# Performance work log

Hardware: AMD Instinct MI355X
Metric: run time of the kernel (lower is better)

The kernel has to match this reference:

```python
import jax, jax.numpy as jnp
import numpy as np

N_NODES = 100000
N_EDGES = 1600000
EMB = 64       # embedding_dim
HID = 128      # hidden_channels
N_GRAPHS = 512
N_TASKS = 128
ATOM_VOCAB = 119
BOND_VOCAB = 16


def setup_inputs() -> dict:
    key = jax.random.key(0)
    ks = jax.random.split(key, 24)
    s = 0.02
    inp = {
        'x_idx': jax.random.randint(ks[0], (N_NODES,), 0, ATOM_VOCAB),
        'edge_index': jax.random.randint(ks[1], (2, N_EDGES), 0, N_NODES),
        'edge_attr_idx': jax.random.randint(ks[2], (N_EDGES,), 0, BOND_VOCAB),
        'batch': jnp.sort(jax.random.randint(ks[3], (N_NODES,), 0, N_GRAPHS)),
        'atom_emb': jax.random.normal(ks[4], (ATOM_VOCAB, EMB), jnp.float32) * s,
        'bond_emb': jax.random.normal(ks[5], (BOND_VOCAB, EMB), jnp.float32) * s,
        'w_edge0': jax.random.normal(ks[6], (EMB, EMB), jnp.float32) * s,
        'b_edge0': jnp.zeros((EMB,), jnp.float32),
        'w1_0': jax.random.normal(ks[7], (EMB, HID), jnp.float32) * s,
        'b1_0': jnp.zeros((HID,), jnp.float32),
        'w2_0': jax.random.normal(ks[8], (HID, HID), jnp.float32) * s,
        'b2_0': jnp.zeros((HID,), jnp.float32),
        'w_edge1': jax.random.normal(ks[9], (EMB, HID), jnp.float32) * s,
        'b_edge1': jnp.zeros((HID,), jnp.float32),
        'w1_1': jax.random.normal(ks[10], (HID, HID), jnp.float32) * s,
        'b1_1': jnp.zeros((HID,), jnp.float32),
        'w2_1': jax.random.normal(ks[11], (HID, HID), jnp.float32) * s,
        'b2_1': jnp.zeros((HID,), jnp.float32),
        'lin1_w': jax.random.normal(ks[12], (HID, HID), jnp.float32) * s,
        'lin1_b': jnp.zeros((HID,), jnp.float32),
        'lin2_w': jax.random.normal(ks[13], (HID, N_TASKS), jnp.float32) * s,
        'lin2_b': jnp.zeros((N_TASKS,), jnp.float32),
    }
    return inp


def _gine_conv(x, e, src, dst, we, be, w1, b1, w2, b2):
    # message: relu(x_j + Linear(edge_attr)); aggregate: scatter-add at dst
    msg = jax.nn.relu(x[src] + e @ we + be)            # [E, in_dim]
    agg = jax.ops.segment_sum(msg, dst, num_segments=N_NODES)
    h = x + agg                                        # (1+eps)*x with eps=0
    h = jax.nn.elu(h @ w1 + b1) @ w2 + b2              # GINE nn MLP
    return jax.nn.elu(h)                               # outer F.elu


def reference(x_idx, edge_index, edge_attr_idx, batch,
              atom_emb, bond_emb,
              w_edge0, b_edge0, w1_0, b1_0, w2_0, b2_0,
              w_edge1, b_edge1, w1_1, b1_1, w2_1, b2_1,
              lin1_w, lin1_b, lin2_w, lin2_b):
    x = atom_emb[x_idx]                                # [N, EMB]
    e = bond_emb[edge_attr_idx]                        # [E, EMB]
    src, dst = edge_index[0], edge_index[1]            # flow: source->target
    x = _gine_conv(x, e, src, dst, w_edge0, b_edge0, w1_0, b1_0, w2_0, b2_0)
    x = _gine_conv(x, e, src, dst, w_edge1, b_edge1, w1_1, b1_1, w2_1, b2_1)
    hg = jax.ops.segment_sum(x, batch, num_segments=N_GRAPHS)  # global_add_pool
    hg = jax.nn.relu(hg @ lin1_w + lin1_b)
    return hg @ lin2_w + lin2_b                        # [G, num_tasks]
```

## Files before the change

kernel.cpp:

```cpp
#include <hip/hip_runtime.h>
#include <hip/hip_bf16.h>

static const int NN = 100000;
static const int NE = 1600000;
static const int NG = 512;
static const int NB = 391;
static const int PS = 4608;
static const int CS = 6400;

typedef __attribute__((ext_vector_type(8))) short shortx8;
typedef __attribute__((ext_vector_type(4))) float floatx4;
typedef __attribute__((ext_vector_type(2))) float floatx2;

__device__ __forceinline__ float bf2f(unsigned short u) {
  union { unsigned int i; float f; } v; v.i = ((unsigned int)u) << 16; return v.f;
}
__device__ __forceinline__ unsigned short f2bf(float f) {
  union { float f; unsigned int i; } v; v.f = f;
  return (unsigned short)((v.i + 0x7FFFu + ((v.i >> 16) & 1u)) >> 16);
}
__device__ __forceinline__ float elu_fast(float v) {
  return v > 0.f ? v : (__builtin_amdgcn_exp2f(v * 1.44269504f) - 1.f);
}
__device__ __forceinline__ floatx2 unpk(unsigned int v) {
  union { unsigned int i; float f; } a, b;
  a.i = v << 16; b.i = v & 0xFFFF0000u;
  floatx2 r; r.x = a.f; r.y = b.f; return r;
}

__global__ void k_prep(const float* __restrict__ bond,
                       const float* __restrict__ we0, const float* __restrict__ be0,
                       const float* __restrict__ we1, const float* __restrict__ be1,
                       const float* __restrict__ atom,
                       float* __restrict__ et1, unsigned short* __restrict__ M0,
                       float* __restrict__ hgf, int* __restrict__ bcursor,
                       unsigned short* __restrict__ x1s,
                       const float* __restrict__ s0, const float* __restrict__ s1,
                       const float* __restrict__ s2, const float* __restrict__ s3,
                       const float* __restrict__ s4, const float* __restrict__ s5,
                       unsigned short* __restrict__ d0, unsigned short* __restrict__ d1,
                       unsigned short* __restrict__ d2, unsigned short* __restrict__ d3,
                       unsigned short* __restrict__ d4, unsigned short* __restrict__ d5) {
  int blk = blockIdx.x, t = threadIdx.x;
  if (blk < 8) {
    int i = blk * 256 + t;
    int b = i >> 7, c = i & 127;
    float acc = be1[c];
    for (int k = 0; k < 64; ++k) acc += bond[b * 64 + k] * we1[k * 128 + c];
    et1[i] = acc;
  } else if (blk < 484) {
    int i = (blk - 8) * 256 + t;
    int c = i & 63, b = (i >> 6) & 15, a = i >> 10;
    float acc = be0[c];
    for (int k = 0; k < 64; ++k) acc += bond[b * 64 + k] * we0[k * 64 + c];
    acc += atom[a * 64 + c];
    M0[i] = f2bf(acc > 0.f ? acc : 0.f);
  } else if (blk < 868) {
    int task = (blk - 484) >> 6;
    int i = ((blk - 484) & 63) * 256 + t;
    const float* w; unsigned short* wz; int K;
    switch (task) {
      case 0: w = s0; wz = d0; K = 64; break;
      case 1: w = s1; wz = d1; K = 128; break;
      case 2: w = s2; wz = d2; K = 128; break;
      case 3: w = s3; wz = d3; K = 128; break;
      case 4: w = s4; wz = d4; K = 128; break;
      default: w = s5; wz = d5; K = 128; break;
    }
    if (i >= K * 128) return;
    int j = i & 7, lane = (i >> 3) & 63, ct = (i >> 9) & 7, s = i >> 12;
    int k = s * 32 + (lane >> 4) * 8 + j;
    int m = ct * 16 + (lane & 15);
    wz[i] = f2bf(w[k * 128 + m]);
  } else if (blk < 884) {
    int base = (blk - 868) * 4096;
#pragma unroll
    for (int k = 0; k < 16; ++k) hgf[base + k * 256 + t] = 0.f;
  } else {
    if (t < NB) bcursor[t] = t * PS;
    int u = t + 256;
    if (u < NB) bcursor[u] = u * PS;
    if (t < 32) ((unsigned int*)(M0 + 1904 * 64))[t] = 0u;
    if (t < 64) ((unsigned int*)(x1s + (size_t)NN * 128))[t] = 0xFF80FF80u;
  }
}

__global__ void k_bin(const int* __restrict__ src, const int* __restrict__ dstp,
                      const int* __restrict__ ea, const int* __restrict__ x_idx,
                      int* __restrict__ bcursor, uint2* __restrict__ pairs) {
  __shared__ int cnt[512];
  __shared__ int incl[512];
  __shared__ int cur[NB];
  __shared__ int rbase[NB];
  __shared__ uint2 stage[4096];
  int t = threadIdx.x;
  int e0 = blockIdx.x * 4096;
  int ecnt = NE - e0; if (ecnt > 4096) ecnt = 4096;
  cnt[t] = 0; cnt[t + 256] = 0;
  __syncthreads();
  for (int k = 0; k < 16; ++k) {
    int i = k * 256 + t;
    if (i < ecnt) atomicAdd(&cnt[dstp[e0 + i] >> 8], 1);
  }
  __syncthreads();
  incl[t] = cnt[t]; incl[t + 256] = cnt[t + 256];
  __syncthreads();
  for (int d = 1; d < 512; d <<= 1) {
    int v0 = (t >= d) ? incl[t - d] : 0;
    int v1 = (t + 256 >= d) ? incl[t + 256 - d] : 0;
    __syncthreads();
    incl[t] += v0; incl[t + 256] += v1;
    __syncthreads();
  }
  if (t < NB) { cur[t] = incl[t] - cnt[t]; if (cnt[t]) rbase[t] = atomicAdd(&bcursor[t], cnt[t]); }
  int u = t + 256;
  if (u < NB) { cur[u] = incl[u] - cnt[u]; if (cnt[u]) rbase[u] = atomicAdd(&bcursor[u], cnt[u]); }
  __syncthreads();
  for (int k = 0; k < 16; ++k) {
    int i = k * 256 + t;
    if (i < ecnt) {
      int e = e0 + i;
      int d = dstp[e];
      int s = src[e];
      unsigned int pk = (unsigned int)s | ((unsigned int)(x_idx[s] * 16 + ea[e]) << 17);
      int p = atomicAdd(&cur[d >> 8], 1);
      stage[p] = make_uint2((unsigned int)d, pk);
    }
  }
  __syncthreads();
  for (int j = t; j < ecnt; j += 256) {
    uint2 p = stage[j];
    int b = (int)(p.x >> 8);
    int excl = incl[b] - cnt[b];
    pairs[rbase[b] + (j - excl)] = p;
  }
}

__global__ void k_fine(const uint2* __restrict__ pairs, const int* __restrict__ bcursor,
                       int* __restrict__ offs, int* __restrict__ cnts,
                       unsigned int* __restrict__ csr0, unsigned int* __restrict__ csr1) {
  __shared__ int cnt[256];
  __shared__ int incl[256];
  __shared__ int cur[256];
  int b = blockIdx.x;
  int t = threadIdx.x;
  int start = b * PS;
  int endv = bcursor[b];
  int cbase = b * CS;
  int base_n = b << 8;
  cnt[t] = 0;
  __syncthreads();
  for (int j = start + t; j < endv; j += 256)
    atomicAdd(&cnt[(int)pairs[j].x - base_n], 1);
  __syncthreads();
  int myc = cnt[t];
  int myp = (myc + 7) & ~7;
  incl[t] = myp;
  __syncthreads();
  for (int d = 1; d < 256; d <<= 1) {
    int v = (t >= d) ? incl[t - d] : 0;
    __syncthreads();
    incl[t] += v;
    __syncthreads();
  }
  int excl = incl[t] - myp;
  cur[t] = excl;
  int node = base_n + t;
  if (node < NN) { offs[node] = cbase + excl; cnts[node] = myc; }
  __syncthreads();
  for (int j = start + t; j < endv; j += 256) {
    uint2 p = pairs[j];
    int pos = cbase + atomicAdd(&cur[(int)p.x - base_n], 1);
    unsigned int pk = p.y;
    unsigned int idx17 = pk >> 17;
    csr0[pos] = idx17 << 7;
    csr1[pos] = ((pk & 0x1FFFFu) << 8) | (idx17 & 15u);
  }
  __syncthreads();
  for (int j = myc; j < myp; ++j) {
    int pos = cbase + excl + j;
    csr0[pos] = (unsigned int)(1904 << 7);
    csr1[pos] = ((unsigned int)NN) << 8;
  }
}

__global__ __launch_bounds__(256) void k_agg0(
    const int* __restrict__ x_idx, const float* __restrict__ atom,
    const unsigned short* __restrict__ M0, const int* __restrict__ offs,
    const int* __restrict__ cnts,
    const unsigned int* __restrict__ csr0, unsigned short* __restrict__ h0) {
  int t = threadIdx.x, lane = t & 63;
  int half = lane >> 5, c = lane & 31;
  int n = __builtin_amdgcn_readfirstlane(blockIdx.x * 4 + (t >> 6));
  if (n >= NN) return;
  int s = offs[n];
  int ep = s + ((cnts[n] + 7) & ~7);
  const char* Mb = (const char*)M0;
  unsigned int voff = (unsigned int)c * 4u;
  floatx2 acc; acc.x = 0.f; acc.y = 0.f;
  if (half == 0) {
    float2 sv = *(const float2*)((const char*)atom +
                                 ((size_t)(unsigned)x_idx[n] << 8) + (size_t)c * 8u);
    acc.x = sv.x; acc.y = sv.y;
  }
  for (int i = s; i < ep; i += 8) {
    unsigned int a0 = csr0[i + 0], b0 = csr0[i + 1];
    unsigned int a1 = csr0[i + 2], b1 = csr0[i + 3];
    unsigned int a2 = csr0[i + 4], b2 = csr0[i + 5];
    unsigned int a3 = csr0[i + 6], b3 = csr0[i + 7];
    unsigned int q0 = half ? b0 : a0, q1 = half ? b1 : a1;
    unsigned int q2 = half ? b2 : a2, q3 = half ? b3 : a3;
    unsigned int v0 = *(const unsigned int*)(Mb + q0 + voff);
    unsigned int v1 = *(const unsigned int*)(Mb + q1 + voff);
    unsigned int v2 = *(const unsigned int*)(Mb + q2 + voff);
    unsigned int v3 = *(const unsigned int*)(Mb + q3 + voff);
    acc = acc + unpk(v0);
    acc = acc + unpk(v1);
    acc = acc + unpk(v2);
    acc = acc + unpk(v3);
  }
  float ax = acc.x + __shfl_xor(acc.x, 32);
  float ay = acc.y + __shfl_xor(acc.y, 32);
  if (half == 0) {
    unsigned int o = (unsigned int)f2bf(ax) | ((unsigned int)f2bf(ay) << 16);
    *(unsigned int*)(h0 + (size_t)n * 64 + c * 2) = o;
  }
}

__global__ __launch_bounds__(256) void k_agg1(
    const unsigned short* __restrict__ x1, const float* __restrict__ et1,
    const int* __restrict__ offs, const int* __restrict__ cnts,
    const unsigned int* __restrict__ csr1, unsigned short* __restrict__ h1) {
  __shared__ float etl[2048];
  int t = threadIdx.x;
#pragma unroll
  for (int k = 0; k < 8; ++k) etl[k * 256 + t] = et1[k * 256 + t];
  __syncthreads();
  int lane = t & 63;
  int n = __builtin_amdgcn_readfirstlane(blockIdx.x * 4 + (t >> 6));
  if (n >= NN) return;
  int s = offs[n];
  int ep = s + ((cnts[n] + 7) & ~7);
  const char* xb = (const char*)x1;
  unsigned int voff = (unsigned int)lane * 4u;
  const char* etb = (const char*)etl + (size_t)lane * 8u;
  unsigned int xv = *(const unsigned int*)(xb + ((size_t)(unsigned)n << 8) + voff);
  floatx2 acc = unpk(xv);
  floatx2 zero2; zero2.x = 0.f; zero2.y = 0.f;
  for (int i = s; i < ep; i += 8) {
    unsigned int q0 = csr1[i + 0], q1 = csr1[i + 1], q2 = csr1[i + 2], q3 = csr1[i + 3];
    unsigned int q4 = csr1[i + 4], q5 = csr1[i + 5], q6 = csr1[i + 6], q7 = csr1[i + 7];
    unsigned int v0 = *(const unsigned int*)(xb + ((q0 & 0xFFFFFF00u) | voff));
    unsigned int v1 = *(const unsigned int*)(xb + ((q1 & 0xFFFFFF00u) | voff));
    unsigned int v2 = *(const unsigned int*)(xb + ((q2 & 0xFFFFFF00u) | voff));
    unsigned int v3 = *(const unsigned int*)(xb + ((q3 & 0xFFFFFF00u) | voff));
    unsigned int v4 = *(const unsigned int*)(xb + ((q4 & 0xFFFFFF00u) | voff));
    unsigned int v5 = *(const unsigned int*)(xb + ((q5 & 0xFFFFFF00u) | voff));
    unsigned int v6 = *(const unsigned int*)(xb + ((q6 & 0xFFFFFF00u) | voff));
    unsigned int v7 = *(const unsigned int*)(xb + ((q7 & 0xFFFFFF00u) | voff));
    floatx2 e0 = *(const floatx2*)(etb + ((q0 & 15u) << 9));
    floatx2 e1 = *(const floatx2*)(etb + ((q1 & 15u) << 9));
    floatx2 e2 = *(const floatx2*)(etb + ((q2 & 15u) << 9));
    floatx2 e3 = *(const floatx2*)(etb + ((q3 & 15u) << 9));
    floatx2 e4 = *(const floatx2*)(etb + ((q4 & 15u) << 9));
    floatx2 e5 = *(const floatx2*)(etb + ((q5 & 15u) << 9));
    floatx2 e6 = *(const floatx2*)(etb + ((q6 & 15u) << 9));
    floatx2 e7 = *(const floatx2*)(etb + ((q7 & 15u) << 9));
    acc = acc + __builtin_elementwise_max(unpk(v0) + e0, zero2);
    acc = acc + __builtin_elementwise_max(unpk(v1) + e1, zero2);
    acc = acc + __builtin_elementwise_max(unpk(v2) + e2, zero2);
    acc = acc + __builtin_elementwise_max(unpk(v3) + e3, zero2);
    acc = acc + __builtin_elementwise_max(unpk(v4) + e4, zero2);
    acc = acc + __builtin_elementwise_max(unpk(v5) + e5, zero2);
    acc = acc + __builtin_elementwise_max(unpk(v6) + e6, zero2);
    acc = acc + __builtin_elementwise_max(unpk(v7) + e7, zero2);
  }
  unsigned int o = (unsigned int)f2bf(acc.x) | ((unsigned int)f2bf(acc.y) << 16);
  *(unsigned int*)(h1 + (size_t)n * 128 + lane * 2) = o;
}

template <int K1>
__global__ __launch_bounds__(256) void k_mlp_t(
    const unsigned short* __restrict__ in,
    const unsigned short* __restrict__ w1z, const float* __restrict__ b1,
    const unsigned short* __restrict__ w2z, const float* __restrict__ b2,
    unsigned short* __restrict__ outb, int N) {
  __shared__ unsigned short tls[4][16][136];
  __shared__ unsigned short b2s[16384];
  int t = threadIdx.x;
  int lane = t & 63;
  int wave = t >> 6;
  int rlo = lane & 15, quad = lane >> 4;

#pragma unroll
  for (int k = 0; k < 8; ++k)
    *(shortx8*)&b2s[(k * 256 + t) * 8] = *(const shortx8*)&w2z[(k * 256 + t) * 8];

  float bm1[8], bm2[8];
#pragma unroll
  for (int ct = 0; ct < 8; ++ct) { bm1[ct] = b1[ct * 16 + rlo]; bm2[ct] = b2[ct * 16 + rlo]; }

  __syncthreads();

#pragma unroll
  for (int t2 = 0; t2 < 2; ++t2) {
    int row0 = blockIdx.x * 128 + t2 * 64 + wave * 16;
    int arow = row0 + rlo;

    floatx4 acc[8];
#pragma unroll
    for (int ct = 0; ct < 8; ++ct) { acc[ct][0]=0.f; acc[ct][1]=0.f; acc[ct][2]=0.f; acc[ct][3]=0.f; }
    const int NS = K1 >> 5;
#pragma unroll
    for (int s = 0; s < NS; ++s) {
      shortx8 a = {0,0,0,0,0,0,0,0};
      if (arow < N) a = *(const shortx8*)(in + (size_t)arow * K1 + s * 32 + quad * 8);
      const unsigned short* wp = w1z + ((size_t)(s * 8) * 64 + lane) * 8;
#pragma unroll
      for (int ct = 0; ct < 8; ++ct) {
        shortx8 b = *(const shortx8*)(wp + ct * 512);
        acc[ct] = __builtin_amdgcn_mfma_f32_16x16x32_bf16(a, b, acc[ct], 0, 0, 0);
      }
    }
#pragma unroll
    for (int ct = 0; ct < 8; ++ct) {
#pragma unroll
      for (int r = 0; r < 4; ++r) {
        float v = elu_fast(acc[ct][r] + bm1[ct]);
        tls[wave][quad * 4 + r][ct * 16 + rlo] = f2bf(v);
      }
    }

    floatx4 acc2[8];
#pragma unroll
    for (int ct = 0; ct < 8; ++ct) { acc2[ct][0]=0.f; acc2[ct][1]=0.f; acc2[ct][2]=0.f; acc2[ct][3]=0.f; }
#pragma unroll
    for (int s = 0; s < 4; ++s) {
      shortx8 a = *(const shortx8*)&tls[wave][rlo][s * 32 + quad * 8];
      const unsigned short* wp = &b2s[((s * 8) * 64 + lane) * 8];
#pragma unroll
      for (int ct = 0; ct < 8; ++ct) {
        shortx8 b = *(const shortx8*)(wp + ct * 512);
        acc2[ct] = __builtin_amdgcn_mfma_f32_16x16x32_bf16(a, b, acc2[ct], 0, 0, 0);
      }
    }
#pragma unroll
    for (int ct = 0; ct < 8; ++ct) {
#pragma unroll
      for (int r = 0; r < 4; ++r) {
        float v = elu_fast(acc2[ct][r] + bm2[ct]);
        tls[wave][quad * 4 + r][ct * 16 + rlo] = f2bf(v);
      }
    }
    int srow = lane >> 2;
    int schunk = lane & 3;
    int grow = row0 + srow;
#pragma unroll
    for (int k = 0; k < 4; ++k) {
      int ch = schunk + k * 4;
      if (grow < N)
        *(shortx8*)(outb + (size_t)grow * 128 + ch * 8) =
            *(const shortx8*)&tls[wave][srow][ch * 8];
    }
  }
}

__global__ __launch_bounds__(256) void k_pool(
    const unsigned short* __restrict__ x2, const int* __restrict__ batch,
    float* __restrict__ hgf) {
  int gt = blockIdx.x * 256 + threadIdx.x;
  int chunk = gt >> 6, lane = gt & 63;
  int n0 = chunk * 32;
  if (n0 >= NN) return;
  int nend = n0 + 32; if (nend > NN) nend = NN;
  float ax = 0.f, ay = 0.f;
  const unsigned short* xp = x2 + lane * 2;
  int gcur = batch[n0];
  for (int n = n0; n < nend; ++n) {
    int g = batch[n];
    if (g != gcur) {
      atomicAdd(&hgf[gcur * 128 + lane * 2], ax);
      atomicAdd(&hgf[gcur * 128 + lane * 2 + 1], ay);
      ax = 0.f; ay = 0.f; gcur = g;
    }
    unsigned int v = *(const unsigned int*)(xp + (size_t)n * 128);
    ax += bf2f((unsigned short)(v & 0xFFFF));
    ay += bf2f((unsigned short)(v >> 16));
  }
  atomicAdd(&hgf[gcur * 128 + lane * 2], ax);
  atomicAdd(&hgf[gcur * 128 + lane * 2 + 1], ay);
}

__global__ void k_head(const float* __restrict__ in,
                       const unsigned short* __restrict__ w1z, const float* __restrict__ b1,
                       const unsigned short* __restrict__ w2z, const float* __restrict__ b2,
                       float* __restrict__ outf, int N) {
  __shared__ unsigned short tls[4][16][136];
  int lane = threadIdx.x & 63;
  int wave = threadIdx.x >> 6;
  int row0 = blockIdx.x * 64 + wave * 16;
  int rlo = lane & 15, quad = lane >> 4;
  int arow = row0 + rlo;
  floatx4 acc[8];
#pragma unroll
  for (int ct = 0; ct < 8; ++ct) { acc[ct][0]=0.f; acc[ct][1]=0.f; acc[ct][2]=0.f; acc[ct][3]=0.f; }
#pragma unroll
  for (int s = 0; s < 4; ++s) {
    shortx8 a = {0,0,0,0,0,0,0,0};
    if (arow < N) {
      const float* rp = in + (size_t)arow * 128 + s * 32 + quad * 8;
      float4 f0 = *(const float4*)rp;
      float4 f1 = *(const float4*)(rp + 4);
      a[0] = (short)f2bf(f0.x); a[1] = (short)f2bf(f0.y);
      a[2] = (short)f2bf(f0.z); a[3] = (short)f2bf(f0.w);
      a[4] = (short)f2bf(f1.x); a[5] = (short)f2bf(f1.y);
      a[6] = (short)f2bf(f1.z); a[7] = (short)f2bf(f1.w);
    }
    const unsigned short* wp = w1z + ((size_t)(s * 8) * 64 + lane) * 8;
#pragma unroll
    for (int ct = 0; ct < 8; ++ct) {
      shortx8 b = *(const shortx8*)(wp + ct * 512);
      acc[ct] = __builtin_amdgcn_mfma_f32_16x16x32_bf16(a, b, acc[ct], 0, 0, 0);
    }
  }
#pragma unroll
  for (int ct = 0; ct < 8; ++ct) {
    float bm = b1[ct * 16 + rlo];
#pragma unroll
    for (int r = 0; r < 4; ++r) {
      float v = acc[ct][r] + bm;
      v = v > 0.f ? v : 0.f;
      tls[wave][quad * 4 + r][ct * 16 + rlo] = f2bf(v);
    }
  }
  __syncthreads();
  floatx4 acc2[8];
#pragma unroll
  for (int ct = 0; ct < 8; ++ct) { acc2[ct][0]=0.f; acc2[ct][1]=0.f; acc2[ct][2]=0.f; acc2[ct][3]=0.f; }
#pragma unroll
  for (int s = 0; s < 4; ++s) {
    shortx8 a = *(const shortx8*)&tls[wave][rlo][s * 32 + quad * 8];
    const unsigned short* wp = w2z + ((size_t)(s * 8) * 64 + lane) * 8;
#pragma unroll
    for (int ct = 0; ct < 8; ++ct) {
      shortx8 b = *(const shortx8*)(wp + ct * 512);
      acc2[ct] = __builtin_amdgcn_mfma_f32_16x16x32_bf16(a, b, acc2[ct], 0, 0, 0);
    }
  }
#pragma unroll
  for (int ct = 0; ct < 8; ++ct) {
    float bm = b2[ct * 16 + rlo];
#pragma unroll
    for (int r = 0; r < 4; ++r) {
      int rr = row0 + quad * 4 + r;
      if (rr < N) outf[(size_t)rr * 128 + ct * 16 + rlo] = acc2[ct][r] + bm;
    }
  }
}

extern "C" void kernel_launch(void* const* d_in, const int* in_sizes, int n_in,
                              void* d_out, int out_size, void* d_ws, size_t ws_size,
                              hipStream_t stream) {
  const int* x_idx  = (const int*)d_in[0];
  const int* e_src  = (const int*)d_in[1];
  const int* e_dst  = e_src + NE;
  const int* e_attr = (const int*)d_in[2];
  const int* batch  = (const int*)d_in[3];
  const float* atom = (const float*)d_in[4];
  const float* bond = (const float*)d_in[5];
  const float* we0  = (const float*)d_in[6];
  const float* be0  = (const float*)d_in[7];
  const float* w1_0 = (const float*)d_in[8];
  const float* b1_0 = (const float*)d_in[9];
  const float* w2_0 = (const float*)d_in[10];
  const float* b2_0 = (const float*)d_in[11];
  const float* we1  = (const float*)d_in[12];
  const float* be1  = (const float*)d_in[13];
  const float* w1_1 = (const float*)d_in[14];
  const float* b1_1 = (const float*)d_in[15];
  const float* w2_1 = (const float*)d_in[16];
  const float* b2_1 = (const float*)d_in[17];
  const float* l1w  = (const float*)d_in[18];
  const float* l1b  = (const float*)d_in[19];
  const float* l2w  = (const float*)d_in[20];
  const float* l2b  = (const float*)d_in[21];

  char* ws = (char*)d_ws;
  size_t off = 0;
  auto alloc = [&](size_t bytes) -> void* {
    void* p = ws + off;
    off = (off + bytes + 255) & ~(size_t)255;
    return p;
  };
  int* bcursor = (int*)alloc((size_t)NB * 4);
  int* offs    = (int*)alloc((size_t)NN * 4);
  int* cnts    = (int*)alloc((size_t)NN * 4);
  float* et1   = (float*)alloc(16 * 128 * 4);
  unsigned short* M0 = (unsigned short*)alloc((size_t)1905 * 64 * 2);
  float* hgf   = (float*)alloc((size_t)NG * 128 * 4);
  unsigned short* w1_0z = (unsigned short*)alloc(64 * 128 * 2);
  unsigned short* w2_0z = (unsigned short*)alloc(128 * 128 * 2);
  unsigned short* w1_1z = (unsigned short*)alloc(128 * 128 * 2);
  unsigned short* w2_1z = (unsigned short*)alloc(128 * 128 * 2);
  unsigned short* l1z   = (unsigned short*)alloc(128 * 128 * 2);
  unsigned short* l2z   = (unsigned short*)alloc(128 * 128 * 2);
  uint2* pairs = (uint2*)alloc((size_t)NB * PS * 8);
  unsigned int* csr0 = (unsigned int*)alloc((size_t)NB * CS * 4);
  unsigned int* csr1 = (unsigned int*)alloc((size_t)NB * CS * 4);
  unsigned short* x1 = (unsigned short*)alloc((size_t)(NN + 1) * 128 * 2);
  unsigned short* h1 = (unsigned short*)alloc((size_t)NN * 128 * 2);
  unsigned short* h0 = (unsigned short*)pairs;
  unsigned short* x2 = h1;

  k_prep<<<885, 256, 0, stream>>>(bond, we0, be0, we1, be1, atom, et1, M0, hgf, bcursor,
                                  x1,
                                  w1_0, w2_0, w1_1, w2_1, l1w, l2w,
                                  w1_0z, w2_0z, w1_1z, w2_1z, l1z, l2z);
  k_bin<<<(NE + 4095) / 4096, 256, 0, stream>>>(e_src, e_dst, e_attr, x_idx, bcursor, pairs);
  k_fine<<<NB, 256, 0, stream>>>(pairs, bcursor, offs, cnts, csr0, csr1);
  k_agg0<<<NN / 4, 256, 0, stream>>>(x_idx, atom, M0, offs, cnts, csr0, h0);
  k_mlp_t<64><<<(NN + 127) / 128, 256, 0, stream>>>(h0, w1_0z, b1_0, w2_0z, b2_0, x1, NN);
  k_agg1<<<NN / 4, 256, 0, stream>>>(x1, et1, offs, cnts, csr1, h1);
  k_mlp_t<128><<<(NN + 127) / 128, 256, 0, stream>>>(h1, w1_1z, b1_1, w2_1z, b2_1, x2, NN);
  k_pool<<<(((NN + 31) / 32) * 64 + 255) / 256, 256, 0, stream>>>(x2, batch, hgf);
  k_head<<<(NG + 63) / 64, 256, 0, stream>>>(hgf, l1z, l1b, l2z, l2b, (float*)d_out, NG);
}
```

Before: 328.1 us.

## Fuse layer-1 aggregation, MLP and global pooling into one kernel

Replaces the separate k_agg1, k_mlp_t<128> and k_pool launches with a single kernel. Each wave aggregates 16 nodes sequentially into LDS, runs both MFMA MLP layers on that tile, and pools the results into per-graph atomics. This removes the round trips of h1 and x2 through global memory and two launches. In exchange the gather phase gets far fewer waves in flight (one wave per 16 nodes instead of one wave per node), which can reduce latency hiding in the memory-bound aggregation. Weights are also read straight from global memory instead of being staged in LDS.

```diff
diff --git a/kernel.cpp b/kernel.cpp
--- a/kernel.cpp
+++ b/kernel.cpp
@@ -227,56 +227,136 @@
   }
 }
 
-__global__ __launch_bounds__(256) void k_agg1(
+__global__ __launch_bounds__(256) void k_fused1(
     const unsigned short* __restrict__ x1, const float* __restrict__ et1,
     const int* __restrict__ offs, const int* __restrict__ cnts,
-    const unsigned int* __restrict__ csr1, unsigned short* __restrict__ h1) {
+    const unsigned int* __restrict__ csr1,
+    const unsigned short* __restrict__ w1z, const float* __restrict__ b1,
+    const unsigned short* __restrict__ w2z, const float* __restrict__ b2,
+    const int* __restrict__ batch, float* __restrict__ hgf) {
   __shared__ float etl[2048];
+  __shared__ unsigned short tls[4][16][136];
   int t = threadIdx.x;
 #pragma unroll
   for (int k = 0; k < 8; ++k) etl[k * 256 + t] = et1[k * 256 + t];
   __syncthreads();
-  int lane = t & 63;
-  int n = __builtin_amdgcn_readfirstlane(blockIdx.x * 4 + (t >> 6));
-  if (n >= NN) return;
-  int s = offs[n];
-  int ep = s + ((cnts[n] + 7) & ~7);
+  int lane = t & 63, wave = t >> 6;
+  int row0 = blockIdx.x * 64 + wave * 16;
   const char* xb = (const char*)x1;
   unsigned int voff = (unsigned int)lane * 4u;
   const char* etb = (const char*)etl + (size_t)lane * 8u;
-  unsigned int xv = *(const unsigned int*)(xb + ((size_t)(unsigned)n << 8) + voff);
-  floatx2 acc = unpk(xv);
   floatx2 zero2; zero2.x = 0.f; zero2.y = 0.f;
-  for (int i = s; i < ep; i += 8) {
-    unsigned int q0 = csr1[i + 0], q1 = csr1[i + 1], q2 = csr1[i + 2], q3 = csr1[i + 3];
-    unsigned int q4 = csr1[i + 4], q5 = csr1[i + 5], q6 = csr1[i + 6], q7 = csr1[i + 7];
-    unsigned int v0 = *(const unsigned int*)(xb + ((q0 & 0xFFFFFF00u) | voff));
-    unsigned int v1 = *(const unsigned int*)(xb + ((q1 & 0xFFFFFF00u) | voff));
-    unsigned int v2 = *(const unsigned int*)(xb + ((q2 & 0xFFFFFF00u) | voff));
-    unsigned int v3 = *(const unsigned int*)(xb + ((q3 & 0xFFFFFF00u) | voff));
-    unsigned int v4 = *(const unsigned int*)(xb + ((q4 & 0xFFFFFF00u) | voff));
-    unsigned int v5 = *(const unsigned int*)(xb + ((q5 & 0xFFFFFF00u) | voff));
-    unsigned int v6 = *(const unsigned int*)(xb + ((q6 & 0xFFFFFF00u) | voff));
-    unsigned int v7 = *(const unsigned int*)(xb + ((q7 & 0xFFFFFF00u) | voff));
-    floatx2 e0 = *(const floatx2*)(etb + ((q0 & 15u) << 9));
-    floatx2 e1 = *(const floatx2*)(etb + ((q1 & 15u) << 9));
-    floatx2 e2 = *(const floatx2*)(etb + ((q2 & 15u) << 9));
-    floatx2 e3 = *(const floatx2*)(etb + ((q3 & 15u) << 9));
-    floatx2 e4 = *(const floatx2*)(etb + ((q4 & 15u) << 9));
-    floatx2 e5 = *(const floatx2*)(etb + ((q5 & 15u) << 9));
-    floatx2 e6 = *(const floatx2*)(etb + ((q6 & 15u) << 9));
-    floatx2 e7 = *(const floatx2*)(etb + ((q7 & 15u) << 9));
-    acc = acc + __builtin_elementwise_max(unpk(v0) + e0, zero2);
-    acc = acc + __builtin_elementwise_max(unpk(v1) + e1, zero2);
-    acc = acc + __builtin_elementwise_max(unpk(v2) + e2, zero2);
-    acc = acc + __builtin_elementwise_max(unpk(v3) + e3, zero2);
-    acc = acc + __builtin_elementwise_max(unpk(v4) + e4, zero2);
-    acc = acc + __builtin_elementwise_max(unpk(v5) + e5, zero2);
-    acc = acc + __builtin_elementwise_max(unpk(v6) + e6, zero2);
-    acc = acc + __builtin_elementwise_max(unpk(v7) + e7, zero2);
-  }
-  unsigned int o = (unsigned int)f2bf(acc.x) | ((unsigned int)f2bf(acc.y) << 16);
-  *(unsigned int*)(h1 + (size_t)n * 128 + lane * 2) = o;
+
+  for (int r = 0; r < 16; ++r) {
+    int n = row0 + r;
+    if (n >= NN) break;
+    int s = offs[n];
+    int ep = s + ((cnts[n] + 7) & ~7);
+    unsigned int xv = *(const unsigned int*)(xb + ((size_t)(unsigned)n << 8) + voff);
+    floatx2 acc = unpk(xv);
+    for (int i = s; i < ep; i += 8) {
+      unsigned int q0 = csr1[i + 0], q1 = csr1[i + 1], q2 = csr1[i + 2], q3 = csr1[i + 3];
+      unsigned int q4 = csr1[i + 4], q5 = csr1[i + 5], q6 = csr1[i + 6], q7 = csr1[i + 7];
+      unsigned int v0 = *(const unsigned int*)(xb + ((q0 & 0xFFFFFF00u) | voff));
+      unsigned int v1 = *(const unsigned int*)(xb + ((q1 & 0xFFFFFF00u) | voff));
+      unsigned int v2 = *(const unsigned int*)(xb + ((q2 & 0xFFFFFF00u) | voff));
+      unsigned int v3 = *(const unsigned int*)(xb + ((q3 & 0xFFFFFF00u) | voff));
+      unsigned int v4 = *(const unsigned int*)(xb + ((q4 & 0xFFFFFF00u) | voff));
+      unsigned int v5 = *(const unsigned int*)(xb + ((q5 & 0xFFFFFF00u) | voff));
+      unsigned int v6 = *(const unsigned int*)(xb + ((q6 & 0xFFFFFF00u) | voff));
+      unsigned int v7 = *(const unsigned int*)(xb + ((q7 & 0xFFFFFF00u) | voff));
+      floatx2 e0 = *(const floatx2*)(etb + ((q0 & 15u) << 9));
+      floatx2 e1 = *(const floatx2*)(etb + ((q1 & 15u) << 9));
+      floatx2 e2 = *(const floatx2*)(etb + ((q2 & 15u) << 9));
+      floatx2 e3 = *(const floatx2*)(etb + ((q3 & 15u) << 9));
+      floatx2 e4 = *(const floatx2*)(etb + ((q4 & 15u) << 9));
+      floatx2 e5 = *(const floatx2*)(etb + ((q5 & 15u) << 9));
+      floatx2 e6 = *(const floatx2*)(etb + ((q6 & 15u) << 9));
+      floatx2 e7 = *(const floatx2*)(etb + ((q7 & 15u) << 9));
+      acc = acc + __builtin_elementwise_max(unpk(v0) + e0, zero2);
+      acc = acc + __builtin_elementwise_max(unpk(v1) + e1, zero2);
+      acc = acc + __builtin_elementwise_max(unpk(v2) + e2, zero2);
+      acc = acc + __builtin_elementwise_max(unpk(v3) + e3, zero2);
+      acc = acc + __builtin_elementwise_max(unpk(v4) + e4, zero2);
+      acc = acc + __builtin_elementwise_max(unpk(v5) + e5, zero2);
+      acc = acc + __builtin_elementwise_max(unpk(v6) + e6, zero2);
+      acc = acc + __builtin_elementwise_max(unpk(v7) + e7, zero2);
+    }
+    unsigned int o = (unsigned int)f2bf(acc.x) | ((unsigned int)f2bf(acc.y) << 16);
+    *(unsigned int*)&tls[wave][r][lane * 2] = o;
+  }
+
+  if (row0 >= NN) return;
+
+  int rlo = lane & 15, quad = lane >> 4;
+  float bm1[8], bm2[8];
+#pragma unroll
+  for (int ct = 0; ct < 8; ++ct) { bm1[ct] = b1[ct * 16 + rlo]; bm2[ct] = b2[ct * 16 + rlo]; }
+
+  floatx4 acc[8];
+#pragma unroll
+  for (int ct = 0; ct < 8; ++ct) { acc[ct][0]=0.f; acc[ct][1]=0.f; acc[ct][2]=0.f; acc[ct][3]=0.f; }
+#pragma unroll
+  for (int s = 0; s < 4; ++s) {
+    shortx8 a = *(const shortx8*)&tls[wave][rlo][s * 32 + quad * 8];
+    const unsigned short* wp = w1z + ((size_t)(s * 8) * 64 + lane) * 8;
+#pragma unroll
+    for (int ct = 0; ct < 8; ++ct) {
+      shortx8 b = *(const shortx8*)(wp + ct * 512);
+      acc[ct] = __builtin_amdgcn_mfma_f32_16x16x32_bf16(a, b, acc[ct], 0, 0, 0);
+    }
+  }
+#pragma unroll
+  for (int ct = 0; ct < 8; ++ct) {
+#pragma unroll
+    for (int r = 0; r < 4; ++r) {
+      float v = elu_fast(acc[ct][r] + bm1[ct]);
+      tls[wave][quad * 4 + r][ct * 16 + rlo] = f2bf(v);
+    }
+  }
+  floatx4 acc2[8];
+#pragma unroll
+  for (int ct = 0; ct < 8; ++ct) { acc2[ct][0]=0.f; acc2[ct][1]=0.f; acc2[ct][2]=0.f; acc2[ct][3]=0.f; }
+#pragma unroll
+  for (int s = 0; s < 4; ++s) {
+    shortx8 a = *(const shortx8*)&tls[wave][rlo][s * 32 + quad * 8];
+    const unsigned short* wp = w2z + ((size_t)(s * 8) * 64 + lane) * 8;
+#pragma unroll
+    for (int ct = 0; ct < 8; ++ct) {
+      shortx8 b = *(const shortx8*)(wp + ct * 512);
+      acc2[ct] = __builtin_amdgcn_mfma_f32_16x16x32_bf16(a, b, acc2[ct], 0, 0, 0);
+    }
+  }
+#pragma unroll
+  for (int ct = 0; ct < 8; ++ct) {
+#pragma unroll
+    for (int r = 0; r < 4; ++r) {
+      float v = elu_fast(acc2[ct][r] + bm2[ct]);
+      tls[wave][quad * 4 + r][ct * 16 + rlo] = f2bf(v);
+    }
+  }
+
+  float px = 0.f, py = 0.f;
+  int gcur = -1;
+  for (int r = 0; r < 16; ++r) {
+    int grow = row0 + r;
+    if (grow >= NN) break;
+    int g = batch[grow];
+    if (g != gcur) {
+      if (gcur >= 0) {
+        atomicAdd(&hgf[gcur * 128 + lane * 2], px);
+        atomicAdd(&hgf[gcur * 128 + lane * 2 + 1], py);
+      }
+      px = 0.f; py = 0.f; gcur = g;
+    }
+    unsigned int v = *(const unsigned int*)&tls[wave][r][lane * 2];
+    floatx2 f = unpk(v);
+    px += f.x; py += f.y;
+  }
+  if (gcur >= 0) {
+    atomicAdd(&hgf[gcur * 128 + lane * 2], px);
+    atomicAdd(&hgf[gcur * 128 + lane * 2 + 1], py);
+  }
 }
 
 template <int K1>
@@ -363,32 +443,6 @@
             *(const shortx8*)&tls[wave][srow][ch * 8];
     }
   }
-}
-
-__global__ __launch_bounds__(256) void k_pool(
-    const unsigned short* __restrict__ x2, const int* __restrict__ batch,
-    float* __restrict__ hgf) {
-  int gt = blockIdx.x * 256 + threadIdx.x;
-  int chunk = gt >> 6, lane = gt & 63;
-  int n0 = chunk * 32;
-  if (n0 >= NN) return;
-  int nend = n0 + 32; if (nend > NN) nend = NN;
-  float ax = 0.f, ay = 0.f;
-  const unsigned short* xp = x2 + lane * 2;
-  int gcur = batch[n0];
-  for (int n = n0; n < nend; ++n) {
-    int g = batch[n];
-    if (g != gcur) {
-      atomicAdd(&hgf[gcur * 128 + lane * 2], ax);
-      atomicAdd(&hgf[gcur * 128 + lane * 2 + 1], ay);
-      ax = 0.f; ay = 0.f; gcur = g;
-    }
-    unsigned int v = *(const unsigned int*)(xp + (size_t)n * 128);
-    ax += bf2f((unsigned short)(v & 0xFFFF));
-    ay += bf2f((unsigned short)(v >> 16));
-  }
-  atomicAdd(&hgf[gcur * 128 + lane * 2], ax);
-  atomicAdd(&hgf[gcur * 128 + lane * 2 + 1], ay);
 }
 
 __global__ void k_head(const float* __restrict__ in,
@@ -508,9 +562,7 @@
   unsigned int* csr0 = (unsigned int*)alloc((size_t)NB * CS * 4);
   unsigned int* csr1 = (unsigned int*)alloc((size_t)NB * CS * 4);
   unsigned short* x1 = (unsigned short*)alloc((size_t)(NN + 1) * 128 * 2);
-  unsigned short* h1 = (unsigned short*)alloc((size_t)NN * 128 * 2);
   unsigned short* h0 = (unsigned short*)pairs;
-  unsigned short* x2 = h1;
 
   k_prep<<<885, 256, 0, stream>>>(bond, we0, be0, we1, be1, atom, et1, M0, hgf, bcursor,
                                   x1,
@@ -520,8 +572,7 @@
   k_fine<<<NB, 256, 0, stream>>>(pairs, bcursor, offs, cnts, csr0, csr1);
   k_agg0<<<NN / 4, 256, 0, stream>>>(x_idx, atom, M0, offs, cnts, csr0, h0);
   k_mlp_t<64><<<(NN + 127) / 128, 256, 0, stream>>>(h0, w1_0z, b1_0, w2_0z, b2_0, x1, NN);
-  k_agg1<<<NN / 4, 256, 0, stream>>>(x1, et1, offs, cnts, csr1, h1);
-  k_mlp_t<128><<<(NN + 127) / 128, 256, 0, stream>>>(h1, w1_1z, b1_1, w2_1z, b2_1, x2, NN);
-  k_pool<<<(((NN + 31) / 32) * 64 + 255) / 256, 256, 0, stream>>>(x2, batch, hgf);
+  k_fused1<<<(NN + 63) / 64, 256, 0, stream>>>(x1, et1, offs, cnts, csr1,
+                                               w1_1z, b1_1, w2_1z, b2_1, batch, hgf);
   k_head<<<(NG + 63) / 64, 256, 0, stream>>>(hgf, l1z, l1b, l2z, l2b, (float*)d_out, NG);
 }
```

Measured after the change: 369.4 us. +12.6%, slower.
